# Optimization experiments

Hardware: AMD Instinct MI355X
Metric: run time of the kernel (lower is better)

Reference implementation:

```python
import jax, jax.numpy as jnp
import numpy as np

DIM = 512
N_HEADS = 8
HEAD_DIM = DIM // N_HEADS
TAU = 0.5
LN_EPS = 1e-5
B, L = 16, 8192


def setup_inputs() -> dict:
    key = jax.random.key(0)
    ks = jax.random.split(key, 12)
    s = 1.0 / np.sqrt(DIM)
    return {
        "Q": jax.random.normal(ks[0], (B, DIM), jnp.float32),
        "K": jax.random.normal(ks[1], (B, L, DIM), jnp.float32),
        "V": jax.random.normal(ks[2], (B, L, DIM), jnp.float32),
        "Wq": jax.random.normal(ks[3], (DIM, DIM), jnp.float32) * s,
        "bq": jnp.zeros((DIM,), jnp.float32),
        "Wk": jax.random.normal(ks[4], (DIM, DIM), jnp.float32) * s,
        "bk": jnp.zeros((DIM,), jnp.float32),
        "Wv": jax.random.normal(ks[5], (DIM, DIM), jnp.float32) * s,
        "bv": jnp.zeros((DIM,), jnp.float32),
        "Wo": jax.random.normal(ks[6], (DIM, DIM), jnp.float32) * s,
        "bo": jnp.zeros((DIM,), jnp.float32),
        "gamma": jnp.ones((DIM,), jnp.float32),
        "beta": jnp.zeros((DIM,), jnp.float32),
    }


def _layer_norm(x, gamma, beta):
    mu = jnp.mean(x, axis=-1, keepdims=True)
    var = jnp.var(x, axis=-1, keepdims=True)
    return (x - mu) * jax.lax.rsqrt(var + LN_EPS) * gamma + beta


def reference(Q, K, V, Wq, bq, Wk, bk, Wv, bv, Wo, bo, gamma, beta):
    Bsz = Q.shape[0]
    # projections
    q = (Q @ Wq + bq).reshape(Bsz, N_HEADS, HEAD_DIM)            # b h d
    k = (K @ Wk + bk).reshape(Bsz, -1, N_HEADS, HEAD_DIM)        # b l h d
    v = (V @ Wv + bv).reshape(Bsz, -1, N_HEADS, HEAD_DIM)        # b l h d
    # scaled dot-product score: single query per head
    scores = jnp.einsum("bhd,blhd->bhl", q, k) / np.sqrt(HEAD_DIM)
    # 'exp' simplex projection = temperature softmax
    weights = jax.nn.softmax(scores / TAU, axis=-1)              # b h l
    ctx = jnp.einsum("bhl,blhd->bhd", weights, v).reshape(Bsz, DIM)
    out = ctx @ Wo + bo                                          # n_heads != 1
    out = _layer_norm(out, gamma, beta)
    return out + Q
```

## Files before the change

### kernel.cpp

```cpp
#include <hip/hip_runtime.h>
#include <math.h>

#define DIM 512
#define NH 8
#define HD 64
#define LSEQ 8192
#define BSZ 16
#define CHUNK 128
#define NCH 64
#define PSTRIDE 4112


__global__ __launch_bounds__(256) void k_qt(const float* __restrict__ Q,
        const float* __restrict__ Wq, const float* __restrict__ bq,
        const float* __restrict__ Wk, float* __restrict__ t_g) {
    int b = blockIdx.x >> 3, h = blockIdx.x & 7;
    int tid = threadIdx.x;
    __shared__ __align__(16) float qs[DIM];
    __shared__ __align__(16) float partial[256];
    __shared__ __align__(16) float qh[HD];
    qs[tid]       = Q[b * DIM + tid];
    qs[tid + 256] = Q[b * DIM + tid + 256];
    __syncthreads();
    int jj = tid & 63, ks = tid >> 6;
    {
        float a = 0.f;
        const float* wp = Wq + (size_t)(ks * 128) * DIM + h * HD + jj;
        const float* qp = qs + ks * 128;
        #pragma unroll 8
        for (int i = 0; i < 128; ++i) a = fmaf(qp[i], wp[(size_t)i * DIM], a);
        partial[tid] = a;
    }
    __syncthreads();
    if (tid < 64)
        qh[tid] = partial[tid] + partial[tid + 64] + partial[tid + 128] +
                  partial[tid + 192] + bq[h * HD + tid];
    __syncthreads();
    #pragma unroll
    for (int rep = 0; rep < 2; ++rep) {
        int i = tid + rep * 256;
        const float4* wk = (const float4*)(Wk + (size_t)i * DIM + h * HD);
        float a = 0.f;
        #pragma unroll
        for (int v = 0; v < 16; ++v) {
            float4 w4 = wk[v];
            a = fmaf(w4.x, qh[v * 4 + 0], a);
            a = fmaf(w4.y, qh[v * 4 + 1], a);
            a = fmaf(w4.z, qh[v * 4 + 2], a);
            a = fmaf(w4.w, qh[v * 4 + 3], a);
        }
        t_g[(size_t)(b * NH + h) * DIM + i] = 0.25f * a;
    }
}

__global__ __launch_bounds__(256) void k_attn(const float* __restrict__ Kin,
        const float* __restrict__ Vin, const float* __restrict__ t_g,
        float* __restrict__ part) {
    int b = blockIdx.x >> 6, chunk = blockIdx.x & 63;
    int tid = threadIdx.x, lane = tid & 63, w = tid >> 6;
    __shared__ __align__(16) float e_lds[CHUNK * 8];
    __shared__ __align__(16) float vstage[8 * DIM];
    __shared__ float wred[32];
    __shared__ float wsum[32];
    float4 ta[8], tb[8];
    #pragma unroll
    for (int h = 0; h < 8; ++h) {
        const float* tp = t_g + (size_t)(b * NH + h) * DIM + lane * 8;
        ta[h] = *(const float4*)tp;
        tb[h] = *(const float4*)(tp + 4);
    }
    const size_t rowbase = (size_t)(b * LSEQ + chunk * CHUNK);
    for (int g = 0; g < 4; ++g) {
        int r0 = w * 32 + g * 8;
        float keep = 0.f;
        #pragma unroll
        for (int i = 0; i < 8; ++i) {
            const float* kp = Kin + (rowbase + r0 + i) * DIM + lane * 8;
            float4 ka = *(const float4*)kp;
            float4 kb = *(const float4*)(kp + 4);
            float s[8];
            #pragma unroll
            for (int h = 0; h < 8; ++h) {
                float p = ka.x * ta[h].x + ka.y * ta[h].y + ka.z * ta[h].z + ka.w * ta[h].w
                        + kb.x * tb[h].x + kb.y * tb[h].y + kb.z * tb[h].z + kb.w * tb[h].w;
                p += __shfl_xor(p, 1);
                p += __shfl_xor(p, 2);
                p += __shfl_xor(p, 4);
                p += __shfl_xor(p, 8);
                p += __shfl_xor(p, 16);
                p += __shfl_xor(p, 32);
                s[h] = p;
            }
            int hh = lane >> 3;
            float sel = s[0];
            sel = (hh == 1) ? s[1] : sel;
            sel = (hh == 2) ? s[2] : sel;
            sel = (hh == 3) ? s[3] : sel;
            sel = (hh == 4) ? s[4] : sel;
            sel = (hh == 5) ? s[5] : sel;
            sel = (hh == 6) ? s[6] : sel;
            sel = (hh == 7) ? s[7] : sel;
            if ((lane & 7) == i) keep = sel;
        }
        e_lds[(r0 + (lane & 7)) * 8 + (lane >> 3)] = keep;
    }
    __syncthreads();
    int h2 = tid & 7, rb = (tid >> 3) * 4;
    float x0 = e_lds[(rb + 0) * 8 + h2], x1 = e_lds[(rb + 1) * 8 + h2];
    float x2 = e_lds[(rb + 2) * 8 + h2], x3 = e_lds[(rb + 3) * 8 + h2];
    float mx = fmaxf(fmaxf(x0, x1), fmaxf(x2, x3));
    mx = fmaxf(mx, __shfl_xor(mx, 8));
    mx = fmaxf(mx, __shfl_xor(mx, 16));
    mx = fmaxf(mx, __shfl_xor(mx, 32));
    if (lane < 8) wred[w * 8 + lane] = mx;
    __syncthreads();
    float m = fmaxf(fmaxf(wred[h2], wred[8 + h2]), fmaxf(wred[16 + h2], wred[24 + h2]));
    float e0 = __expf(x0 - m), e1 = __expf(x1 - m);
    float e2 = __expf(x2 - m), e3 = __expf(x3 - m);
    e_lds[(rb + 0) * 8 + h2] = e0;
    e_lds[(rb + 1) * 8 + h2] = e1;
    e_lds[(rb + 2) * 8 + h2] = e2;
    e_lds[(rb + 3) * 8 + h2] = e3;
    float sm = e0 + e1 + e2 + e3;
    sm += __shfl_xor(sm, 8);
    sm += __shfl_xor(sm, 16);
    sm += __shfl_xor(sm, 32);
    if (lane < 8) wsum[w * 8 + lane] = sm;
    __syncthreads();
    int r = tid >> 7, col = (tid & 127) << 2;
    float4 a0 = {0,0,0,0}, a1 = {0,0,0,0}, a2 = {0,0,0,0}, a3 = {0,0,0,0};
    float4 a4 = {0,0,0,0}, a5 = {0,0,0,0}, a6 = {0,0,0,0}, a7 = {0,0,0,0};
    #pragma unroll 4
    for (int j = r; j < CHUNK; j += 2) {
        const float* vp = Vin + (rowbase + j) * DIM + col;
        float4 vv = *(const float4*)vp;
        float4 wa = *(const float4*)&e_lds[j * 8];
        float4 wb = *(const float4*)&e_lds[j * 8 + 4];
        a0.x = fmaf(wa.x, vv.x, a0.x); a0.y = fmaf(wa.x, vv.y, a0.y);
        a0.z = fmaf(wa.x, vv.z, a0.z); a0.w = fmaf(wa.x, vv.w, a0.w);
        a1.x = fmaf(wa.y, vv.x, a1.x); a1.y = fmaf(wa.y, vv.y, a1.y);
        a1.z = fmaf(wa.y, vv.z, a1.z); a1.w = fmaf(wa.y, vv.w, a1.w);
        a2.x = fmaf(wa.z, vv.x, a2.x); a2.y = fmaf(wa.z, vv.y, a2.y);
        a2.z = fmaf(wa.z, vv.z, a2.z); a2.w = fmaf(wa.z, vv.w, a2.w);
        a3.x = fmaf(wa.w, vv.x, a3.x); a3.y = fmaf(wa.w, vv.y, a3.y);
        a3.z = fmaf(wa.w, vv.z, a3.z); a3.w = fmaf(wa.w, vv.w, a3.w);
        a4.x = fmaf(wb.x, vv.x, a4.x); a4.y = fmaf(wb.x, vv.y, a4.y);
        a4.z = fmaf(wb.x, vv.z, a4.z); a4.w = fmaf(wb.x, vv.w, a4.w);
        a5.x = fmaf(wb.y, vv.x, a5.x); a5.y = fmaf(wb.y, vv.y, a5.y);
        a5.z = fmaf(wb.y, vv.z, a5.z); a5.w = fmaf(wb.y, vv.w, a5.w);
        a6.x = fmaf(wb.z, vv.x, a6.x); a6.y = fmaf(wb.z, vv.y, a6.y);
        a6.z = fmaf(wb.z, vv.z, a6.z); a6.w = fmaf(wb.z, vv.w, a6.w);
        a7.x = fmaf(wb.w, vv.x, a7.x); a7.y = fmaf(wb.w, vv.y, a7.y);
        a7.z = fmaf(wb.w, vv.z, a7.z); a7.w = fmaf(wb.w, vv.w, a7.w);
    }
    __syncthreads();
    if (r == 1) {
        *(float4*)&vstage[0 * DIM + col] = a0; *(float4*)&vstage[1 * DIM + col] = a1;
        *(float4*)&vstage[2 * DIM + col] = a2; *(float4*)&vstage[3 * DIM + col] = a3;
        *(float4*)&vstage[4 * DIM + col] = a4; *(float4*)&vstage[5 * DIM + col] = a5;
        *(float4*)&vstage[6 * DIM + col] = a6; *(float4*)&vstage[7 * DIM + col] = a7;
    }
    __syncthreads();
    float* pout = part + (size_t)(b * NCH + chunk) * PSTRIDE;
    if (r == 0) {
        float4 o;
        #define EMIT(H, A) \
            o = *(const float4*)&vstage[H * DIM + col]; \
            o.x += A.x; o.y += A.y; o.z += A.z; o.w += A.w; \
            *(float4*)&pout[H * DIM + col] = o;
        EMIT(0, a0) EMIT(1, a1) EMIT(2, a2) EMIT(3, a3)
        EMIT(4, a4) EMIT(5, a5) EMIT(6, a6) EMIT(7, a7)
        #undef EMIT
    }
    if (tid < 8) {
        float mm = fmaxf(fmaxf(wred[tid], wred[8 + tid]), fmaxf(wred[16 + tid], wred[24 + tid]));
        pout[4096 + tid] = mm;
        pout[4104 + tid] = wsum[tid] + wsum[8 + tid] + wsum[16 + tid] + wsum[24 + tid];
    }
}

__global__ __launch_bounds__(256) void k_uctx(const float* __restrict__ part,
        const float* __restrict__ Wv, const float* __restrict__ bv,
        float* __restrict__ ctx) {
    int b = blockIdx.x >> 3, h = blockIdx.x & 7;
    int tid = threadIdx.x;
    __shared__ __align__(16) float alphas[NCH];
    __shared__ __align__(16) float u_lds[DIM];
    __shared__ __align__(16) float red4[256];
    __shared__ float sinv_s;
    if (tid < 64) {
        const float* pm = part + (size_t)(b * NCH + tid) * PSTRIDE;
        float mv = pm[4096 + h], sv = pm[4104 + h];
        float M = mv;
        #pragma unroll
        for (int d = 1; d < 64; d <<= 1) M = fmaxf(M, __shfl_xor(M, d));
        float al = __expf(mv - M);
        alphas[tid] = al;
        float c = al * sv;
        #pragma unroll
        for (int d = 1; d < 64; d <<= 1) c += __shfl_xor(c, d);
        if (tid == 0) sinv_s = 1.f / c;
    }
    __syncthreads();
    float sinv = sinv_s;
    float u0 = 0.f, u1 = 0.f;
    #pragma unroll 4
    for (int c = 0; c < NCH; ++c) {
        const float* pu = part + (size_t)(b * NCH + c) * PSTRIDE + h * DIM;
        float al = alphas[c];
        u0 = fmaf(al, pu[tid], u0);
        u1 = fmaf(al, pu[tid + 256], u1);
    }
    u_lds[tid]       = u0 * sinv;
    u_lds[tid + 256] = u1 * sinv;
    __syncthreads();
    int jj = tid & 63, ks = tid >> 6;
    float a = 0.f;
    const float* wp = Wv + (size_t)(ks * 128) * DIM + h * HD + jj;
    const float* up = u_lds + ks * 128;
    #pragma unroll 8
    for (int i = 0; i < 128; ++i) a = fmaf(up[i], wp[(size_t)i * DIM], a);
    red4[tid] = a;
    __syncthreads();
    if (tid < 64)
        ctx[b * DIM + h * HD + tid] = red4[tid] + red4[tid + 64] +
            red4[tid + 128] + red4[tid + 192] + bv[h * HD + tid];
}

__global__ __launch_bounds__(256) void k_oproj(const float* __restrict__ ctx,
        const float* __restrict__ Wo, float* __restrict__ po) {
    int b = blockIdx.x >> 3, ks = blockIdx.x & 7;
    int tid = threadIdx.x;
    __shared__ float cs[64];
    if (tid < 64) cs[tid] = ctx[b * DIM + ks * 64 + tid];
    __syncthreads();
    float a0 = 0.f, a1 = 0.f;
    const float* wp = Wo + (size_t)(ks * 64) * DIM;
    #pragma unroll 8
    for (int i = 0; i < 64; ++i) {
        float c = cs[i];
        a0 = fmaf(c, wp[(size_t)i * DIM + tid], a0);
        a1 = fmaf(c, wp[(size_t)i * DIM + tid + 256], a1);
    }
    po[(size_t)(b * 8 + ks) * DIM + tid]       = a0;
    po[(size_t)(b * 8 + ks) * DIM + tid + 256] = a1;
}

__global__ __launch_bounds__(256) void k_ln(const float* __restrict__ po,
        const float* __restrict__ bo, const float* __restrict__ gamma,
        const float* __restrict__ beta, const float* __restrict__ Qin,
        float* __restrict__ out) {
    int b = blockIdx.x, tid = threadIdx.x;
    float o0 = bo[tid], o1 = bo[tid + 256];
    #pragma unroll
    for (int ks = 0; ks < 8; ++ks) {
        o0 += po[(size_t)(b * 8 + ks) * DIM + tid];
        o1 += po[(size_t)(b * 8 + ks) * DIM + tid + 256];
    }
    float s = o0 + o1, sq = o0 * o0 + o1 * o1;
    #pragma unroll
    for (int d = 1; d < 64; d <<= 1) { s += __shfl_xor(s, d); sq += __shfl_xor(sq, d); }
    __shared__ float rs[4], rq[4];
    int lane = tid & 63, wave = tid >> 6;
    if (lane == 0) { rs[wave] = s; rq[wave] = sq; }
    __syncthreads();
    s  = rs[0] + rs[1] + rs[2] + rs[3];
    sq = rq[0] + rq[1] + rq[2] + rq[3];
    float mu = s * (1.f / DIM);
    float var = sq * (1.f / DIM) - mu * mu;
    float rstd = rsqrtf(var + 1e-5f);
    int j0 = tid, j1 = tid + 256;
    out[b * DIM + j0] = (o0 - mu) * rstd * gamma[j0] + beta[j0] + Qin[b * DIM + j0];
    out[b * DIM + j1] = (o1 - mu) * rstd * gamma[j1] + beta[j1] + Qin[b * DIM + j1];
}

extern "C" void kernel_launch(void* const* d_in, const int* in_sizes, int n_in,
                              void* d_out, int out_size, void* d_ws, size_t ws_size,
                              hipStream_t stream) {
    const float* Q     = (const float*)d_in[0];
    const float* K     = (const float*)d_in[1];
    const float* V     = (const float*)d_in[2];
    const float* Wq    = (const float*)d_in[3];
    const float* bq    = (const float*)d_in[4];
    const float* Wk    = (const float*)d_in[5];
    const float* Wv    = (const float*)d_in[7];
    const float* bv    = (const float*)d_in[8];
    const float* Wo    = (const float*)d_in[9];
    const float* bo    = (const float*)d_in[10];
    const float* gamma = (const float*)d_in[11];
    const float* beta  = (const float*)d_in[12];
    float* ws   = (float*)d_ws;
    float* t_g  = ws;
    float* part = ws + 65536;
    float* ctx  = ws + 4276224;
    float* po   = ws + 4284416;
    float* out  = (float*)d_out;

    k_qt   <<<128,  256, 0, stream>>>(Q, Wq, bq, Wk, t_g);
    k_attn <<<1024, 256, 0, stream>>>(K, V, t_g, part);
    k_uctx <<<128,  256, 0, stream>>>(part, Wv, bv, ctx);
    k_oproj<<<128,  256, 0, stream>>>(ctx, Wo, po);
    k_ln   <<<16,   256, 0, stream>>>(po, bo, gamma, beta, Q, out);
}
```

Baseline: 569.8 us.

## Cut score shuffles, widen uctx to 512 threads, fuse oproj with layernorm

Measured after the change: 589.4 us. 1.03x slower.

```diff
diff --git a/kernel.cpp b/kernel.cpp
--- a/kernel.cpp
+++ b/kernel.cpp
@@ -78,28 +78,28 @@
             const float* kp = Kin + (rowbase + r0 + i) * DIM + lane * 8;
             float4 ka = *(const float4*)kp;
             float4 kb = *(const float4*)(kp + 4);
-            float s[8];
+            float p[8];
             #pragma unroll
             for (int h = 0; h < 8; ++h) {
-                float p = ka.x * ta[h].x + ka.y * ta[h].y + ka.z * ta[h].z + ka.w * ta[h].w
+                float q = ka.x * ta[h].x + ka.y * ta[h].y + ka.z * ta[h].z + ka.w * ta[h].w
                         + kb.x * tb[h].x + kb.y * tb[h].y + kb.z * tb[h].z + kb.w * tb[h].w;
-                p += __shfl_xor(p, 1);
-                p += __shfl_xor(p, 2);
-                p += __shfl_xor(p, 4);
-                p += __shfl_xor(p, 8);
-                p += __shfl_xor(p, 16);
-                p += __shfl_xor(p, 32);
-                s[h] = p;
+                q += __shfl_xor(q, 8);
+                q += __shfl_xor(q, 16);
+                q += __shfl_xor(q, 32);
+                p[h] = q;
             }
             int hh = lane >> 3;
-            float sel = s[0];
-            sel = (hh == 1) ? s[1] : sel;
-            sel = (hh == 2) ? s[2] : sel;
-            sel = (hh == 3) ? s[3] : sel;
-            sel = (hh == 4) ? s[4] : sel;
-            sel = (hh == 5) ? s[5] : sel;
-            sel = (hh == 6) ? s[6] : sel;
-            sel = (hh == 7) ? s[7] : sel;
+            float sel = p[0];
+            sel = (hh == 1) ? p[1] : sel;
+            sel = (hh == 2) ? p[2] : sel;
+            sel = (hh == 3) ? p[3] : sel;
+            sel = (hh == 4) ? p[4] : sel;
+            sel = (hh == 5) ? p[5] : sel;
+            sel = (hh == 6) ? p[6] : sel;
+            sel = (hh == 7) ? p[7] : sel;
+            sel += __shfl_xor(sel, 1);
+            sel += __shfl_xor(sel, 2);
+            sel += __shfl_xor(sel, 4);
             if ((lane & 7) == i) keep = sel;
         }
         e_lds[(r0 + (lane & 7)) * 8 + (lane >> 3)] = keep;
@@ -179,14 +179,14 @@
     }
 }
 
-__global__ __launch_bounds__(256) void k_uctx(const float* __restrict__ part,
+__global__ __launch_bounds__(512) void k_uctx(const float* __restrict__ part,
         const float* __restrict__ Wv, const float* __restrict__ bv,
         float* __restrict__ ctx) {
     int b = blockIdx.x >> 3, h = blockIdx.x & 7;
     int tid = threadIdx.x;
     __shared__ __align__(16) float alphas[NCH];
     __shared__ __align__(16) float u_lds[DIM];
-    __shared__ __align__(16) float red4[256];
+    __shared__ __align__(16) float red[512];
     __shared__ float sinv_s;
     if (tid < 64) {
         const float* pm = part + (size_t)(b * NCH + tid) * PSTRIDE;
@@ -202,76 +202,55 @@
         if (tid == 0) sinv_s = 1.f / c;
     }
     __syncthreads();
-    float sinv = sinv_s;
-    float u0 = 0.f, u1 = 0.f;
+    float u0 = 0.f;
     #pragma unroll 4
     for (int c = 0; c < NCH; ++c) {
         const float* pu = part + (size_t)(b * NCH + c) * PSTRIDE + h * DIM;
-        float al = alphas[c];
-        u0 = fmaf(al, pu[tid], u0);
-        u1 = fmaf(al, pu[tid + 256], u1);
-    }
-    u_lds[tid]       = u0 * sinv;
-    u_lds[tid + 256] = u1 * sinv;
+        u0 = fmaf(alphas[c], pu[tid], u0);
+    }
+    u_lds[tid] = u0 * sinv_s;
     __syncthreads();
     int jj = tid & 63, ks = tid >> 6;
     float a = 0.f;
-    const float* wp = Wv + (size_t)(ks * 128) * DIM + h * HD + jj;
-    const float* up = u_lds + ks * 128;
+    const float* wp = Wv + (size_t)(ks * 64) * DIM + h * HD + jj;
+    const float* up = u_lds + ks * 64;
     #pragma unroll 8
-    for (int i = 0; i < 128; ++i) a = fmaf(up[i], wp[(size_t)i * DIM], a);
-    red4[tid] = a;
-    __syncthreads();
-    if (tid < 64)
-        ctx[b * DIM + h * HD + tid] = red4[tid] + red4[tid + 64] +
-            red4[tid + 128] + red4[tid + 192] + bv[h * HD + tid];
-}
-
-__global__ __launch_bounds__(256) void k_oproj(const float* __restrict__ ctx,
-        const float* __restrict__ Wo, float* __restrict__ po) {
-    int b = blockIdx.x >> 3, ks = blockIdx.x & 7;
-    int tid = threadIdx.x;
-    __shared__ float cs[64];
-    if (tid < 64) cs[tid] = ctx[b * DIM + ks * 64 + tid];
-    __syncthreads();
-    float a0 = 0.f, a1 = 0.f;
-    const float* wp = Wo + (size_t)(ks * 64) * DIM;
+    for (int i = 0; i < 64; ++i) a = fmaf(up[i], wp[(size_t)i * DIM], a);
+    red[tid] = a;
+    __syncthreads();
+    if (tid < 64) {
+        float rsum = red[tid]       + red[tid + 64]  + red[tid + 128] + red[tid + 192]
+                   + red[tid + 256] + red[tid + 320] + red[tid + 384] + red[tid + 448];
+        ctx[b * DIM + h * HD + tid] = rsum + bv[h * HD + tid];
+    }
+}
+
+__global__ __launch_bounds__(512) void k_oln(const float* __restrict__ ctx,
+        const float* __restrict__ Wo, const float* __restrict__ bo,
+        const float* __restrict__ gamma, const float* __restrict__ beta,
+        const float* __restrict__ Qin, float* __restrict__ out) {
+    int b = blockIdx.x, tid = threadIdx.x;
+    __shared__ __align__(16) float cs[DIM];
+    __shared__ float rs[8], rq[8];
+    cs[tid] = ctx[b * DIM + tid];
+    __syncthreads();
+    float o = bo[tid];
+    const float* wp = Wo + tid;
     #pragma unroll 8
-    for (int i = 0; i < 64; ++i) {
-        float c = cs[i];
-        a0 = fmaf(c, wp[(size_t)i * DIM + tid], a0);
-        a1 = fmaf(c, wp[(size_t)i * DIM + tid + 256], a1);
-    }
-    po[(size_t)(b * 8 + ks) * DIM + tid]       = a0;
-    po[(size_t)(b * 8 + ks) * DIM + tid + 256] = a1;
-}
-
-__global__ __launch_bounds__(256) void k_ln(const float* __restrict__ po,
-        const float* __restrict__ bo, const float* __restrict__ gamma,
-        const float* __restrict__ beta, const float* __restrict__ Qin,
-        float* __restrict__ out) {
-    int b = blockIdx.x, tid = threadIdx.x;
-    float o0 = bo[tid], o1 = bo[tid + 256];
-    #pragma unroll
-    for (int ks = 0; ks < 8; ++ks) {
-        o0 += po[(size_t)(b * 8 + ks) * DIM + tid];
-        o1 += po[(size_t)(b * 8 + ks) * DIM + tid + 256];
-    }
-    float s = o0 + o1, sq = o0 * o0 + o1 * o1;
+    for (int k = 0; k < DIM; ++k) o = fmaf(cs[k], wp[(size_t)k * DIM], o);
+    float s = o, sq = o * o;
     #pragma unroll
     for (int d = 1; d < 64; d <<= 1) { s += __shfl_xor(s, d); sq += __shfl_xor(sq, d); }
-    __shared__ float rs[4], rq[4];
-    int lane = tid & 63, wave = tid >> 6;
-    if (lane == 0) { rs[wave] = s; rq[wave] = sq; }
-    __syncthreads();
-    s  = rs[0] + rs[1] + rs[2] + rs[3];
-    sq = rq[0] + rq[1] + rq[2] + rq[3];
+    int lane = tid & 63, wv = tid >> 6;
+    if (lane == 0) { rs[wv] = s; rq[wv] = sq; }
+    __syncthreads();
+    s = 0.f; sq = 0.f;
+    #pragma unroll
+    for (int i = 0; i < 8; ++i) { s += rs[i]; sq += rq[i]; }
     float mu = s * (1.f / DIM);
     float var = sq * (1.f / DIM) - mu * mu;
     float rstd = rsqrtf(var + 1e-5f);
-    int j0 = tid, j1 = tid + 256;
-    out[b * DIM + j0] = (o0 - mu) * rstd * gamma[j0] + beta[j0] + Qin[b * DIM + j0];
-    out[b * DIM + j1] = (o1 - mu) * rstd * gamma[j1] + beta[j1] + Qin[b * DIM + j1];
+    out[b * DIM + tid] = (o - mu) * rstd * gamma[tid] + beta[tid] + Qin[b * DIM + tid];
 }
 
 extern "C" void kernel_launch(void* const* d_in, const int* in_sizes, int n_in,
@@ -293,12 +272,10 @@
     float* t_g  = ws;
     float* part = ws + 65536;
     float* ctx  = ws + 4276224;
-    float* po   = ws + 4284416;
     float* out  = (float*)d_out;
 
     k_qt   <<<128,  256, 0, stream>>>(Q, Wq, bq, Wk, t_g);
     k_attn <<<1024, 256, 0, stream>>>(K, V, t_g, part);
-    k_uctx <<<128,  256, 0, stream>>>(part, Wv, bv, ctx);
-    k_oproj<<<128,  256, 0, stream>>>(ctx, Wo, po);
-    k_ln   <<<16,   256, 0, stream>>>(po, bo, gamma, beta, Q, out);
-}
+    k_uctx <<<128,  512, 0, stream>>>(part, Wv, bv, ctx);
+    k_oln  <<<16,   512, 0, stream>>>(ctx, Wo, bo, gamma, beta, Q, out);
+}
```
